# Kernel optimization log

Hardware: AMD Instinct MI355X
Metric: run time of the kernel (lower is better)

Reference implementation:

```python
import jax, jax.numpy as jnp
import numpy as np

B, K, N, D, H, DOUT = 16, 8, 196, 768, 3072, 768


def setup_inputs() -> dict:
    key = jax.random.key(0)
    ks = jax.random.split(key, 5)
    scale_w1 = 1.0 / np.sqrt(D)
    scale_w2 = 1.0 / np.sqrt(H)
    return {
        "slots": jax.random.normal(ks[0], (B, K, D), dtype=jnp.float32),
        "pos_embed": jax.random.normal(ks[1], (N, D), dtype=jnp.float32) * 0.02,
        "map_alpha": jax.random.normal(ks[2], (N, DOUT), dtype=jnp.float32) * 0.02,
        "W1": jax.random.normal(ks[3], (D, H), dtype=jnp.float32) * scale_w1,
        "b1": jnp.zeros((H,), dtype=jnp.float32),
        "W2": jax.random.normal(ks[4], (H, DOUT), dtype=jnp.float32) * scale_w2,
        "b2": jnp.zeros((DOUT,), dtype=jnp.float32),
    }


def reference(slots, pos_embed, map_alpha, W1, b1, W2, b2):
    b, k, d = slots.shape
    n = pos_embed.shape[0]
    # broadcast slots over patches and add positional embedding: (B,K,N,D)
    tokens = slots[:, :, None, :] + pos_embed[None, None, :, :]
    # 2-layer MLP with ReLU
    h = jax.nn.relu(jnp.einsum('bknd,dh->bknh', tokens, W1) + b1)
    y_k = jnp.einsum('bknh,ho->bkno', h, W2) + b2  # (B,K,N,DOUT)
    # softmax over K of map_alpha expanded over (B,K); identical across K -> uniform 1/K,
    # computed explicitly for faithfulness to the original module
    m_k = jax.nn.softmax(jnp.broadcast_to(map_alpha[None, None, :, :], (b, k, n, map_alpha.shape[1])), axis=1)
    y = jnp.einsum('bknd,bknd->bnd', y_k, m_k)
    return y
```

## Files before the change

kernel.cpp:

```cpp
#include <hip/hip_runtime.h>
#include <hip/hip_bf16.h>
#include <stdint.h>


typedef __attribute__((ext_vector_type(8))) short bf16x8;
typedef __attribute__((ext_vector_type(4))) float f32x4;

#define AS1 __attribute__((address_space(1)))
#define AS3 __attribute__((address_space(3)))

#define WAIT_VM(N) asm volatile("s_waitcnt vmcnt(" #N ")" ::: "memory")
#define BAR()      asm volatile("s_barrier" ::: "memory")
#define BAR_LDS()  asm volatile("s_waitcnt lgkmcnt(0)\ns_barrier" ::: "memory")

static __device__ __forceinline__ void gld_lds16(const void* g, void* l) {
    __builtin_amdgcn_global_load_lds((const AS1 unsigned int*)g,
                                     (AS3 unsigned int*)l, 16, 0, 0);
}

static __device__ __forceinline__ unsigned short f2bf(float f) {
    union { float f; unsigned int u; } v; v.f = f;
    unsigned int u = v.u;
    return (unsigned short)((u + 0x7fffu + ((u >> 16) & 1u)) >> 16);
}

__global__ void k_prep(const float* __restrict__ W1, unsigned short* __restrict__ W1t,
                       const float* __restrict__ S, const float* __restrict__ P,
                       unsigned short* __restrict__ A1) {
    int idx = blockIdx.x * blockDim.x + threadIdx.x;
    const int C1n = 96 * 3072;
    const int PKn = 96 * 384;
    if (idx < C1n) {
        int r  = idx % 3072;
        int kc = idx / 3072;
        unsigned int po[4];
        #pragma unroll
        for (int j = 0; j < 4; ++j) {
            unsigned short lo = f2bf(W1[(size_t)(kc * 8 + 2 * j) * 3072 + r]);
            unsigned short hi = f2bf(W1[(size_t)(kc * 8 + 2 * j + 1) * 3072 + r]);
            po[j] = (unsigned int)lo | ((unsigned int)hi << 16);
        }
        size_t dst = ((size_t)(r >> 6) * 12 + (kc >> 3)) * 4096
                   + (size_t)((kc & 7) * 64 + (r & 63)) * 8;
        *(uint4*)(W1t + dst) = make_uint4(po[0], po[1], po[2], po[3]);
    } else if (idx < C1n + PKn) {
        int t = idx - C1n;
        int r  = t % 384;
        int kc = t / 384;
        uint4 o = make_uint4(0u, 0u, 0u, 0u);
        if (r < 324) {
            const float* src = (r < 128) ? (S + (size_t)r * 768 + kc * 8)
                                         : (P + (size_t)(r - 128) * 768 + kc * 8);
            float4 a = *(const float4*)(src);
            float4 b = *(const float4*)(src + 4);
            o.x = (unsigned int)f2bf(a.x) | ((unsigned int)f2bf(a.y) << 16);
            o.y = (unsigned int)f2bf(a.z) | ((unsigned int)f2bf(a.w) << 16);
            o.z = (unsigned int)f2bf(b.x) | ((unsigned int)f2bf(b.y) << 16);
            o.w = (unsigned int)f2bf(b.z) | ((unsigned int)f2bf(b.w) << 16);
        }
        size_t dst = ((size_t)(r >> 6) * 12 + (kc >> 3)) * 4096
                   + (size_t)((kc & 7) * 64 + (r & 63)) * 8;
        *(uint4*)(A1 + dst) = o;
    }
}

__launch_bounds__(256)
__global__ void k_gemm1_w2t(const unsigned short* __restrict__ A,
                            const unsigned short* __restrict__ Bt,
                            float* __restrict__ C,
                            const float* __restrict__ W2,
                            unsigned short* __restrict__ W2t) {
    const int tid = threadIdx.x;
    if (blockIdx.x >= 288) {
        int idx = (blockIdx.x - 288) * 256 + tid;
        int r  = idx % 768;
        int kc = idx / 768;
        unsigned int po[4];
        #pragma unroll
        for (int j = 0; j < 4; ++j) {
            unsigned short lo = f2bf(W2[(size_t)(kc * 8 + 2 * j) * 768 + r]);
            unsigned short hi = f2bf(W2[(size_t)(kc * 8 + 2 * j + 1) * 768 + r]);
            po[j] = (unsigned int)lo | ((unsigned int)hi << 16);
        }
        size_t dst = ((size_t)(r >> 6) * 48 + (kc >> 3)) * 4096
                   + (size_t)((kc & 7) * 64 + (r & 63)) * 8;
        *(uint4*)(W2t + dst) = make_uint4(po[0], po[1], po[2], po[3]);
        return;
    }

    __shared__ unsigned short sm[3 * 8192];
    const int lane = tid & 63;
    const int wave = tid >> 6;
    const int wm = wave >> 1, wn = wave & 1;
    const int q = lane >> 4, l16 = lane & 15;

    const int id = blockIdx.x;
    const int j  = id >> 3;
    const int nt = (id & 7) * 6 + j % 6;
    const int rt = j / 6;

    const unsigned short* Ab = A  + (size_t)rt * 12 * 4096;
    const unsigned short* Bb = Bt + (size_t)nt * 12 * 4096;

    f32x4 acc[2][2] = {};
    const int offA = (wm * 32 + l16) * 8;
    const int offB = 4096 + (wn * 32 + l16) * 8;

    auto stage = [&](int i, unsigned short* d) {
        const unsigned short* Ag = Ab + (size_t)i * 4096;
        const unsigned short* Bg = Bb + (size_t)i * 4096;
        gld_lds16(Ag + tid * 8,        d + tid * 8);
        gld_lds16(Ag + 2048 + tid * 8, d + 2048 + tid * 8);
        gld_lds16(Bg + tid * 8,        d + 4096 + tid * 8);
        gld_lds16(Bg + 2048 + tid * 8, d + 6144 + tid * 8);
    };
    auto compute = [&](const unsigned short* buf) {
        #pragma unroll
        for (int ks = 0; ks < 2; ++ks) {
            const int ko = (ks * 4 + q) * 512;
            bf16x8 af0 = *(const bf16x8*)(buf + ko + offA);
            bf16x8 af1 = *(const bf16x8*)(buf + ko + offA + 128);
            bf16x8 bf0 = *(const bf16x8*)(buf + ko + offB);
            bf16x8 bf1 = *(const bf16x8*)(buf + ko + offB + 128);
            acc[0][0] = __builtin_amdgcn_mfma_f32_16x16x32_bf16(af0, bf0, acc[0][0], 0, 0, 0);
            acc[0][1] = __builtin_amdgcn_mfma_f32_16x16x32_bf16(af0, bf1, acc[0][1], 0, 0, 0);
            acc[1][0] = __builtin_amdgcn_mfma_f32_16x16x32_bf16(af1, bf0, acc[1][0], 0, 0, 0);
            acc[1][1] = __builtin_amdgcn_mfma_f32_16x16x32_bf16(af1, bf1, acc[1][1], 0, 0, 0);
        }
    };

    unsigned short* s0 = sm;
    unsigned short* s1 = sm + 8192;
    unsigned short* s2 = sm + 16384;

    stage(0, s0);
    stage(1, s1);
    for (int i = 0; i < 12; i += 3) {
        stage(i + 2, s2); WAIT_VM(8);
        BAR(); compute(s0); BAR_LDS();
        if (i + 3 < 12) { stage(i + 3, s0); WAIT_VM(8); } else { WAIT_VM(4); }
        BAR(); compute(s1); BAR_LDS();
        if (i + 4 < 12) { stage(i + 4, s1); WAIT_VM(8); }
        else if (i + 3 < 12) { WAIT_VM(4); }
        else { WAIT_VM(0); }
        BAR(); compute(s2);
        if (i + 3 < 12) BAR_LDS();
    }

    const int row0 = rt * 64 + wm * 32;
    const int col0 = nt * 64 + wn * 32;
    #pragma unroll
    for (int ii = 0; ii < 2; ++ii) {
        #pragma unroll
        for (int jj = 0; jj < 2; ++jj) {
            int col = col0 + jj * 16 + l16;
            #pragma unroll
            for (int r = 0; r < 4; ++r) {
                int row = row0 + ii * 16 + q * 4 + r;
                if (row < 324) C[(size_t)row * 3072 + col] = acc[ii][jj][r];
            }
        }
    }
}

__global__ void k_hbar(const float* __restrict__ C1, const float* __restrict__ b1,
                       unsigned short* __restrict__ Hb) {
    const int bid  = blockIdx.x;
    const int tid  = threadIdx.x;
    const int bx   = bid % 49;
    const int yq   = bid / 49;
    const int lane = tid & 63;
    const int wv   = tid >> 6;
    const int hc   = yq * 4 + wv;
    const int h0   = hc * 8;
    const int bn   = bx * 64 + lane;
    const int b    = bn / 196;
    const int n    = bn - b * 196;
    const float* prow = C1 + (size_t)(128 + n) * 3072 + h0;
    float4 pA = *(const float4*)(prow);
    float4 pB = *(const float4*)(prow + 4);
    float4 bA = *(const float4*)(b1 + h0);
    float4 bB = *(const float4*)(b1 + h0 + 4);
    float pb[8] = { pA.x + bA.x, pA.y + bA.y, pA.z + bA.z, pA.w + bA.w,
                    pB.x + bB.x, pB.y + bB.y, pB.z + bB.z, pB.w + bB.w };
    float acc[8] = {};
    #pragma unroll
    for (int k = 0; k < 8; ++k) {
        const float* srow = C1 + (size_t)(b * 8 + k) * 3072 + h0;
        float4 sA_ = *(const float4*)(srow);
        float4 sB_ = *(const float4*)(srow + 4);
        acc[0] += fmaxf(sA_.x + pb[0], 0.f);
        acc[1] += fmaxf(sA_.y + pb[1], 0.f);
        acc[2] += fmaxf(sA_.z + pb[2], 0.f);
        acc[3] += fmaxf(sA_.w + pb[3], 0.f);
        acc[4] += fmaxf(sB_.x + pb[4], 0.f);
        acc[5] += fmaxf(sB_.y + pb[5], 0.f);
        acc[6] += fmaxf(sB_.z + pb[6], 0.f);
        acc[7] += fmaxf(sB_.w + pb[7], 0.f);
    }
    unsigned int w0 = (unsigned int)f2bf(acc[0] * 0.125f) | ((unsigned int)f2bf(acc[1] * 0.125f) << 16);
    unsigned int w1 = (unsigned int)f2bf(acc[2] * 0.125f) | ((unsigned int)f2bf(acc[3] * 0.125f) << 16);
    unsigned int w2 = (unsigned int)f2bf(acc[4] * 0.125f) | ((unsigned int)f2bf(acc[5] * 0.125f) << 16);
    unsigned int w3 = (unsigned int)f2bf(acc[6] * 0.125f) | ((unsigned int)f2bf(acc[7] * 0.125f) << 16);
    size_t dst = ((size_t)bx * 48 + (hc >> 3)) * 4096
               + (size_t)((hc & 7) * 64 + lane) * 8;
    *(uint4*)(Hb + dst) = make_uint4(w0, w1, w2, w3);
}

__launch_bounds__(512)
__global__ void k_gemm2(const unsigned short* __restrict__ Hb,
                        const unsigned short* __restrict__ W2t,
                        const float* __restrict__ b2, float* __restrict__ out) {
    __shared__ unsigned short sm[3 * 8192];

    const int tid  = threadIdx.x;
    const int lane = tid & 63;
    const int wave = tid >> 6;
    const int wm = wave >> 1, wn = wave & 1;
    const int q = lane >> 4, l16 = lane & 15;

    const int id = blockIdx.x;
    int rt, nt;
    if (id < 576) { rt = (id & 7) + 8 * ((id >> 3) % 6); nt = (id >> 3) / 6; }
    else          { rt = 48; nt = id - 576; }

    const unsigned short* Ab = Hb  + (size_t)rt * 48 * 4096;
    const unsigned short* Bb = W2t + (size_t)nt * 48 * 4096;

    f32x4 acc[2] = {};

    auto stage = [&](int i, unsigned short* d) {
        gld_lds16(Ab + (size_t)i * 4096 + tid * 8, d + tid * 8);
        gld_lds16(Bb + (size_t)i * 4096 + tid * 8, d + 4096 + tid * 8);
    };

    const int offA = (wm * 16 + l16) * 8;
    const int offB = 4096 + (wn * 32 + l16) * 8;
    auto compute = [&](const unsigned short* buf) {
        #pragma unroll
        for (int ks = 0; ks < 2; ++ks) {
            const int ko = (ks * 4 + q) * 512;
            bf16x8 af  = *(const bf16x8*)(buf + ko + offA);
            bf16x8 bf0 = *(const bf16x8*)(buf + ko + offB);
            bf16x8 bf1 = *(const bf16x8*)(buf + ko + offB + 128);
            acc[0] = __builtin_amdgcn_mfma_f32_16x16x32_bf16(af, bf0, acc[0], 0, 0, 0);
            acc[1] = __builtin_amdgcn_mfma_f32_16x16x32_bf16(af, bf1, acc[1], 0, 0, 0);
        }
    };

    unsigned short* s0 = sm;
    unsigned short* s1 = sm + 8192;
    unsigned short* s2 = sm + 16384;

    stage(0, s0);
    stage(1, s1);
    for (int i = 0; i < 48; i += 3) {
        stage(i + 2, s2); WAIT_VM(4);
        BAR(); compute(s0); BAR_LDS();
        if (i + 3 < 48) { stage(i + 3, s0); WAIT_VM(4); } else { WAIT_VM(2); }
        BAR(); compute(s1); BAR_LDS();
        if (i + 4 < 48) { stage(i + 4, s1); WAIT_VM(4); }
        else if (i + 3 < 48) { WAIT_VM(2); }
        else { WAIT_VM(0); }
        BAR(); compute(s2);
        if (i + 3 < 48) BAR_LDS();
    }

    const int row0 = rt * 64 + wm * 16;
    const int col0 = nt * 64 + wn * 32;
    #pragma unroll
    for (int jj = 0; jj < 2; ++jj) {
        int col = col0 + jj * 16 + l16;
        float bv = b2[col];
        #pragma unroll
        for (int r = 0; r < 4; ++r) {
            int row = row0 + q * 4 + r;
            out[(size_t)row * 768 + col] = acc[jj][r] + bv;
        }
    }
}

extern "C" void kernel_launch(void* const* d_in, const int* in_sizes, int n_in,
                              void* d_out, int out_size, void* d_ws, size_t ws_size,
                              hipStream_t stream) {
    const float* slots  = (const float*)d_in[0];
    const float* pos    = (const float*)d_in[1];
    const float* W1     = (const float*)d_in[3];
    const float* b1     = (const float*)d_in[4];
    const float* W2     = (const float*)d_in[5];
    const float* b2     = (const float*)d_in[6];
    float* out = (float*)d_out;

    size_t off = 0;
    auto alloc = [&](size_t bytes) {
        void* p = (char*)d_ws + off;
        off += (bytes + 255) & ~(size_t)255;
        return p;
    };
    unsigned short* W1t = (unsigned short*)alloc((size_t)3072 * 768 * 2);
    unsigned short* W2t = (unsigned short*)alloc((size_t)768 * 3072 * 2);
    unsigned short* A1  = (unsigned short*)alloc((size_t)384 * 768 * 2);
    float*          C1  = (float*)alloc((size_t)384 * 3072 * 4);
    unsigned short* Hb  = (unsigned short*)alloc((size_t)49 * 48 * 4096 * 2);

    k_prep<<<1296, 256, 0, stream>>>(W1, W1t, slots, pos, A1);
    k_gemm1_w2t<<<1440, 256, 0, stream>>>(A1, W1t, C1, W2, W2t);
    k_hbar<<<4704, 256, 0, stream>>>(C1, b1, Hb);
    k_gemm2<<<588, 512, 0, stream>>>(Hb, W2t, b2, out);
}
```

Measured before the change: 130.4 us.

## Split K across wave groups in gemm2 with 2x2 register tiles and LDS reduction

Each gemm2 block's 8 waves are reorganized into two K-groups of four waves. Each wave now computes a 32x32 output tile (2x2 MFMA accumulators) over half of each K-chunk instead of a 16x32 tile over the whole chunk. This raises fragment reuse per LDS read, with 4 LDS loads for 4 MFMAs versus 6 for 4 before. The two groups' partial sums are then combined through shared memory, which adds an extra barrier and an LDS round trip at the end.

```diff
diff --git a/kernel.cpp b/kernel.cpp
--- a/kernel.cpp
+++ b/kernel.cpp
@@ -216,7 +216,9 @@
     const int tid  = threadIdx.x;
     const int lane = tid & 63;
     const int wave = tid >> 6;
-    const int wm = wave >> 1, wn = wave & 1;
+    const int kg = wave >> 2;
+    const int w  = wave & 3;
+    const int wm = w >> 1, wn = w & 1;
     const int q = lane >> 4, l16 = lane & 15;
 
     const int id = blockIdx.x;
@@ -227,25 +229,25 @@
     const unsigned short* Ab = Hb  + (size_t)rt * 48 * 4096;
     const unsigned short* Bb = W2t + (size_t)nt * 48 * 4096;
 
-    f32x4 acc[2] = {};
+    f32x4 acc[2][2] = {};
 
     auto stage = [&](int i, unsigned short* d) {
         gld_lds16(Ab + (size_t)i * 4096 + tid * 8, d + tid * 8);
         gld_lds16(Bb + (size_t)i * 4096 + tid * 8, d + 4096 + tid * 8);
     };
 
-    const int offA = (wm * 16 + l16) * 8;
+    const int offA = (wm * 32 + l16) * 8;
     const int offB = 4096 + (wn * 32 + l16) * 8;
+    const int ko   = (kg * 4 + q) * 512;
     auto compute = [&](const unsigned short* buf) {
-        #pragma unroll
-        for (int ks = 0; ks < 2; ++ks) {
-            const int ko = (ks * 4 + q) * 512;
-            bf16x8 af  = *(const bf16x8*)(buf + ko + offA);
-            bf16x8 bf0 = *(const bf16x8*)(buf + ko + offB);
-            bf16x8 bf1 = *(const bf16x8*)(buf + ko + offB + 128);
-            acc[0] = __builtin_amdgcn_mfma_f32_16x16x32_bf16(af, bf0, acc[0], 0, 0, 0);
-            acc[1] = __builtin_amdgcn_mfma_f32_16x16x32_bf16(af, bf1, acc[1], 0, 0, 0);
-        }
+        bf16x8 af0 = *(const bf16x8*)(buf + ko + offA);
+        bf16x8 af1 = *(const bf16x8*)(buf + ko + offA + 128);
+        bf16x8 bf0 = *(const bf16x8*)(buf + ko + offB);
+        bf16x8 bf1 = *(const bf16x8*)(buf + ko + offB + 128);
+        acc[0][0] = __builtin_amdgcn_mfma_f32_16x16x32_bf16(af0, bf0, acc[0][0], 0, 0, 0);
+        acc[0][1] = __builtin_amdgcn_mfma_f32_16x16x32_bf16(af0, bf1, acc[0][1], 0, 0, 0);
+        acc[1][0] = __builtin_amdgcn_mfma_f32_16x16x32_bf16(af1, bf0, acc[1][0], 0, 0, 0);
+        acc[1][1] = __builtin_amdgcn_mfma_f32_16x16x32_bf16(af1, bf1, acc[1][1], 0, 0, 0);
     };
 
     unsigned short* s0 = sm;
@@ -266,16 +268,38 @@
         if (i + 3 < 48) BAR_LDS();
     }
 
-    const int row0 = rt * 64 + wm * 16;
+    float* smf = (float*)sm;
+    __syncthreads();
+    if (kg == 1) {
+        #pragma unroll
+        for (int ii = 0; ii < 2; ++ii)
+            #pragma unroll
+            for (int jj = 0; jj < 2; ++jj)
+                *(f32x4*)(smf + ((size_t)((w * 4 + ii * 2 + jj) * 64 + lane)) * 4) = acc[ii][jj];
+    }
+    __syncthreads();
+    if (kg == 1) return;
+    #pragma unroll
+    for (int ii = 0; ii < 2; ++ii)
+        #pragma unroll
+        for (int jj = 0; jj < 2; ++jj) {
+            f32x4 p = *(const f32x4*)(smf + ((size_t)((w * 4 + ii * 2 + jj) * 64 + lane)) * 4);
+            acc[ii][jj] += p;
+        }
+
+    const int row0 = rt * 64 + wm * 32;
     const int col0 = nt * 64 + wn * 32;
     #pragma unroll
-    for (int jj = 0; jj < 2; ++jj) {
-        int col = col0 + jj * 16 + l16;
-        float bv = b2[col];
-        #pragma unroll
-        for (int r = 0; r < 4; ++r) {
-            int row = row0 + q * 4 + r;
-            out[(size_t)row * 768 + col] = acc[jj][r] + bv;
+    for (int ii = 0; ii < 2; ++ii) {
+        #pragma unroll
+        for (int jj = 0; jj < 2; ++jj) {
+            int col = col0 + jj * 16 + l16;
+            float bv = b2[col];
+            #pragma unroll
+            for (int r = 0; r < 4; ++r) {
+                int row = row0 + ii * 16 + q * 4 + r;
+                out[(size_t)row * 768 + col] = acc[ii][jj][r] + bv;
+            }
         }
     }
 }
```

New measurement: 129.0 us. About the same (-1.1%).

## Enlarge GEMM2 block tile to 128x128 with 4x2 MFMA fragments per wave

Applied to the files above, without the earlier changes.

The second GEMM's block tile grows from 64x64 to 128x128, so each wave computes a 64x32 sub-tile with eight accumulators instead of two. This raises arithmetic intensity per LDS/global load and removes redundant re-reads of Hb and W2t across blocks. The trade-off is only 150 blocks, which may leave many of the 256 CUs idle. It also doubles LDS use to 96 KB per block and pads the last row tile with a duplicated block, guarded on store.

```diff
diff --git a/kernel.cpp b/kernel.cpp
--- a/kernel.cpp
+++ b/kernel.cpp
@@ -211,71 +211,84 @@
 __global__ void k_gemm2(const unsigned short* __restrict__ Hb,
                         const unsigned short* __restrict__ W2t,
                         const float* __restrict__ b2, float* __restrict__ out) {
-    __shared__ unsigned short sm[3 * 8192];
+    __shared__ unsigned short sm[3 * 16384];
 
     const int tid  = threadIdx.x;
     const int lane = tid & 63;
     const int wave = tid >> 6;
-    const int wm = wave >> 1, wn = wave & 1;
+    const int wm2 = wave >> 2;
+    const int wn2 = wave & 3;
     const int q = lane >> 4, l16 = lane & 15;
 
-    const int id = blockIdx.x;
-    int rt, nt;
-    if (id < 576) { rt = (id & 7) + 8 * ((id >> 3) % 6); nt = (id >> 3) / 6; }
-    else          { rt = 48; nt = id - 576; }
-
-    const unsigned short* Ab = Hb  + (size_t)rt * 48 * 4096;
-    const unsigned short* Bb = W2t + (size_t)nt * 48 * 4096;
-
-    f32x4 acc[2] = {};
+    const int id  = blockIdx.x;
+    const int rt2 = id % 25;
+    const int nt2 = id / 25;
+
+    const int bxA0 = rt2 * 2;
+    const int bxA1 = (rt2 * 2 + 1 < 49) ? rt2 * 2 + 1 : 48;
+    const unsigned short* A0g = Hb  + (size_t)bxA0 * 48 * 4096;
+    const unsigned short* A1g = Hb  + (size_t)bxA1 * 48 * 4096;
+    const unsigned short* B0g = W2t + (size_t)(nt2 * 2)     * 48 * 4096;
+    const unsigned short* B1g = W2t + (size_t)(nt2 * 2 + 1) * 48 * 4096;
+
+    f32x4 acc[4][2] = {};
 
     auto stage = [&](int i, unsigned short* d) {
-        gld_lds16(Ab + (size_t)i * 4096 + tid * 8, d + tid * 8);
-        gld_lds16(Bb + (size_t)i * 4096 + tid * 8, d + 4096 + tid * 8);
-    };
-
-    const int offA = (wm * 16 + l16) * 8;
-    const int offB = 4096 + (wn * 32 + l16) * 8;
+        const size_t o = (size_t)i * 4096;
+        gld_lds16(A0g + o + tid * 8, d + tid * 8);
+        gld_lds16(A1g + o + tid * 8, d + 4096  + tid * 8);
+        gld_lds16(B0g + o + tid * 8, d + 8192  + tid * 8);
+        gld_lds16(B1g + o + tid * 8, d + 12288 + tid * 8);
+    };
+
+    const int offA = wm2 * 4096 + l16 * 8;
+    const int offB = 8192 + (wn2 >> 1) * 4096 + ((wn2 & 1) * 32 + l16) * 8;
     auto compute = [&](const unsigned short* buf) {
         #pragma unroll
         for (int ks = 0; ks < 2; ++ks) {
             const int ko = (ks * 4 + q) * 512;
-            bf16x8 af  = *(const bf16x8*)(buf + ko + offA);
-            bf16x8 bf0 = *(const bf16x8*)(buf + ko + offB);
-            bf16x8 bf1 = *(const bf16x8*)(buf + ko + offB + 128);
-            acc[0] = __builtin_amdgcn_mfma_f32_16x16x32_bf16(af, bf0, acc[0], 0, 0, 0);
-            acc[1] = __builtin_amdgcn_mfma_f32_16x16x32_bf16(af, bf1, acc[1], 0, 0, 0);
+            bf16x8 bf0 = *(const bf16x8*)(buf + offB + ko);
+            bf16x8 bf1 = *(const bf16x8*)(buf + offB + ko + 128);
+            #pragma unroll
+            for (int rf = 0; rf < 4; ++rf) {
+                bf16x8 af = *(const bf16x8*)(buf + offA + ko + rf * 128);
+                acc[rf][0] = __builtin_amdgcn_mfma_f32_16x16x32_bf16(af, bf0, acc[rf][0], 0, 0, 0);
+                acc[rf][1] = __builtin_amdgcn_mfma_f32_16x16x32_bf16(af, bf1, acc[rf][1], 0, 0, 0);
+            }
         }
     };
 
     unsigned short* s0 = sm;
-    unsigned short* s1 = sm + 8192;
-    unsigned short* s2 = sm + 16384;
+    unsigned short* s1 = sm + 16384;
+    unsigned short* s2 = sm + 32768;
 
     stage(0, s0);
     stage(1, s1);
     for (int i = 0; i < 48; i += 3) {
-        stage(i + 2, s2); WAIT_VM(4);
+        stage(i + 2, s2); WAIT_VM(8);
         BAR(); compute(s0); BAR_LDS();
-        if (i + 3 < 48) { stage(i + 3, s0); WAIT_VM(4); } else { WAIT_VM(2); }
+        if (i + 3 < 48) { stage(i + 3, s0); WAIT_VM(8); } else { WAIT_VM(4); }
         BAR(); compute(s1); BAR_LDS();
-        if (i + 4 < 48) { stage(i + 4, s1); WAIT_VM(4); }
-        else if (i + 3 < 48) { WAIT_VM(2); }
+        if (i + 4 < 48) { stage(i + 4, s1); WAIT_VM(8); }
+        else if (i + 3 < 48) { WAIT_VM(4); }
         else { WAIT_VM(0); }
         BAR(); compute(s2);
         if (i + 3 < 48) BAR_LDS();
     }
 
-    const int row0 = rt * 64 + wm * 16;
-    const int col0 = nt * 64 + wn * 32;
+    const int row0 = rt2 * 128 + wm2 * 64;
+    const int col0 = nt2 * 128 + wn2 * 32;
     #pragma unroll
-    for (int jj = 0; jj < 2; ++jj) {
-        int col = col0 + jj * 16 + l16;
-        float bv = b2[col];
-        #pragma unroll
-        for (int r = 0; r < 4; ++r) {
-            int row = row0 + q * 4 + r;
-            out[(size_t)row * 768 + col] = acc[jj][r] + bv;
+    for (int rf = 0; rf < 4; ++rf) {
+        #pragma unroll
+        for (int cf = 0; cf < 2; ++cf) {
+            int col = col0 + cf * 16 + l16;
+            float bv = b2[col];
+            #pragma unroll
+            for (int r = 0; r < 4; ++r) {
+                int row = row0 + rf * 16 + q * 4 + r;
+                if (row < 3136) out[(size_t)row * 768 + col] = acc[rf][cf][r] + bv;
+            }
         }
     }
 }
@@ -306,5 +319,5 @@
     k_prep<<<1296, 256, 0, stream>>>(W1, W1t, slots, pos, A1);
     k_gemm1_w2t<<<1440, 256, 0, stream>>>(A1, W1t, C1, W2, W2t);
     k_hbar<<<4704, 256, 0, stream>>>(C1, b1, Hb);
-    k_gemm2<<<588, 512, 0, stream>>>(Hb, W2t, b2, out);
-}
+    k_gemm2<<<150, 512, 0, stream>>>(Hb, W2t, b2, out);
+}
```

Result: slower. 134.7 us (+3.3%).
